# Kernel tuning notes

Measured on AMD Instinct MI355X. Metric: run time of the kernel, lower is better.

The kernel has to match this reference:

```python
import jax, jax.numpy as jnp
import numpy as np

B, G, DIN, DOUT = 4096, 16, 512, 512

def setup_inputs() -> dict:
    key = jax.random.key(0)
    kx, kw, kb = jax.random.split(key, 3)
    x = jax.random.normal(kx, (B, G, DIN), dtype=jnp.float32)
    # per-group nn.Linear weight: [G, dim_out, dim_in] (torch layout)
    W = jax.random.normal(kw, (G, DOUT, DIN), dtype=jnp.float32) * (1.0 / np.sqrt(DIN))
    b = jax.random.normal(kb, (G, DOUT), dtype=jnp.float32) * 0.01
    return {"x": x, "W": W, "b": b}

def reference(x, W, b):
    # MultiLinear: independent Linear per group g; y[..., g, :] = x[..., g, :] @ W[g].T + b[g]
    # Fused as a single batched GEMM over the group dimension.
    y = jnp.einsum('bgi,goi->bgo', x, W)  # [B, G, DOUT]
    return y + b
```

## Files before the change

kernel.cpp:

```cpp
#include <hip/hip_runtime.h>
#include <hip/hip_bf16.h>


#define BATCH 4096
#define NGRP  16
#define DIN   512
#define DOUT  512

#define BM 128
#define BN 512
#define BK 64
#define NT (DIN / BK)

typedef __bf16 bf16x8 __attribute__((ext_vector_type(8)));
typedef float  f32x4  __attribute__((ext_vector_type(4)));
typedef const __attribute__((address_space(1))) void gas_void;
typedef __attribute__((address_space(3))) void las_void;

__global__ __launch_bounds__(256)
void wcvt_kernel(const float* __restrict__ W, __bf16* __restrict__ Wb) {
    const int i = (blockIdx.x * 256 + threadIdx.x) * 8;
    f32x4 a = *(const f32x4*)(W + i);
    f32x4 b = *(const f32x4*)(W + i + 4);
    bf16x8 v;
#pragma unroll
    for (int j = 0; j < 4; ++j) { v[j] = (__bf16)a[j]; v[j + 4] = (__bf16)b[j]; }
    *(bf16x8*)(Wb + i) = v;
}

__global__ __launch_bounds__(512, 2)
void MultiLinear_48498770706571_kernel(const float* __restrict__ X,
                                       const __bf16* __restrict__ Wb,
                                       const float* __restrict__ Bias,
                                       float* __restrict__ Y) {
    const int bid = (blockIdx.x & 7) * 64 + (blockIdx.x >> 3);
    const int g   = bid >> 5;
    const int mt  = bid & 31;
    const int bm0 = mt * BM;

    __shared__ __bf16 As[2][BM * BK];
    __shared__ __bf16 BsF[2][BN * BK];

    const int tid  = threadIdx.x;
    const int lane = tid & 63;
    const int w    = tid >> 6;
    const int wn   = w * 64;
    const int l15  = lane & 15;
    const int q    = lane >> 4;

    const int srow = tid >> 2;
    const int sc2  = (tid & 3) * 2;
    const float* pA = X + (size_t)(bm0 + srow) * (NGRP * DIN) + g * DIN + (tid & 3) * 16;

    const int drow_l = lane >> 3;
    const int dch    = lane & 7;
    const __bf16* wbase = Wb + (size_t)g * (DOUT * DIN);

    f32x4 ra[4];

#define ISSUE_A(k0)                                                        \
    do {                                                                   \
        const f32x4* qa = (const f32x4*)(pA + (k0));                       \
        ra[0] = qa[0]; ra[1] = qa[1]; ra[2] = qa[2]; ra[3] = qa[3];        \
    } while (0)

#define CVT_WRITE_A(buf)                                                   \
    do {                                                                   \
        bf16x8 v0, v1;                                                     \
        _Pragma("unroll")                                                  \
        for (int j = 0; j < 4; ++j) {                                      \
            v0[j] = (__bf16)ra[0][j]; v0[j + 4] = (__bf16)ra[1][j];        \
            v1[j] = (__bf16)ra[2][j]; v1[j + 4] = (__bf16)ra[3][j];        \
        }                                                                  \
        const int s = srow & 7;                                            \
        __bf16* base = &As[buf][srow * BK];                                \
        *(bf16x8*)&base[((sc2 ^ s) << 3)]       = v0;                      \
        *(bf16x8*)&base[(((sc2 + 1) ^ s) << 3)] = v1;                      \
    } while (0)

#define DMA_B(kt, buf)                                                     \
    do {                                                                   \
        const size_t k0 = (size_t)(kt) * BK;                               \
        _Pragma("unroll")                                                  \
        for (int qq = 0; qq < 8; ++qq) {                                   \
            const int row = (w << 6) + (qq << 3) + drow_l;                 \
            const __bf16* gp = wbase + (size_t)row * DIN + k0              \
                               + ((dch ^ (row & 7)) << 3);                 \
            __builtin_amdgcn_global_load_lds(                              \
                (gas_void*)gp,                                             \
                (las_void*)&BsF[buf][(w << 12) + (qq << 9)], 16, 0, 0);    \
        }                                                                  \
    } while (0)

#define COMPUTE(buf)                                                       \
    do {                                                                   \
        _Pragma("unroll")                                                  \
        for (int kk = 0; kk < 2; ++kk) {                                   \
            bf16x8 af[8], bfr[4];                                          \
            _Pragma("unroll")                                              \
            for (int mi = 0; mi < 8; ++mi) {                               \
                const int row = mi * 16 + l15;                             \
                const int ch  = ((kk << 2) + q) ^ (row & 7);               \
                af[mi] = *(const bf16x8*)&As[buf][row * BK + (ch << 3)];   \
            }                                                              \
            _Pragma("unroll")                                              \
            for (int ni = 0; ni < 4; ++ni) {                               \
                const int brow = wn + ni * 16 + l15;                       \
                const int ch = ((kk << 2) + q) ^ (brow & 7);               \
                bfr[ni] = *(const bf16x8*)&BsF[buf][brow * BK + (ch << 3)]; \
            }                                                              \
            _Pragma("unroll")                                              \
            for (int mi = 0; mi < 8; ++mi)                                 \
                _Pragma("unroll")                                          \
                for (int ni = 0; ni < 4; ++ni)                             \
                    acc[mi][ni] = __builtin_amdgcn_mfma_f32_16x16x32_bf16( \
                        af[mi], bfr[ni], acc[mi][ni], 0, 0, 0);            \
        }                                                                  \
    } while (0)

    f32x4 acc[8][4];
#pragma unroll
    for (int mi = 0; mi < 8; ++mi)
#pragma unroll
        for (int ni = 0; ni < 4; ++ni) acc[mi][ni] = f32x4{0.f, 0.f, 0.f, 0.f};

    ISSUE_A(0);
    DMA_B(0, 0);
    CVT_WRITE_A(0);
    ISSUE_A(BK);

    for (int kt = 0; kt < NT; ++kt) {
        const int cur = kt & 1;
        if (kt + 1 < NT)
            asm volatile("s_waitcnt vmcnt(4)" ::: "memory");
        else
            asm volatile("s_waitcnt vmcnt(0)" ::: "memory");
        asm volatile("s_waitcnt lgkmcnt(0)" ::: "memory");
        __builtin_amdgcn_s_barrier();

        if (kt + 1 < NT) DMA_B(kt + 1, cur ^ 1);

        COMPUTE(cur);

        if (kt + 1 < NT) {
            CVT_WRITE_A(cur ^ 1);
            if (kt + 2 < NT) ISSUE_A((kt + 2) * BK);
        }
    }

    const int r0 = (lane >> 4) * 4;
    const int c  = lane & 15;
    float bias_n[4];
#pragma unroll
    for (int ni = 0; ni < 4; ++ni)
        bias_n[ni] = Bias[g * DOUT + wn + ni * 16 + c];
#pragma unroll
    for (int mi = 0; mi < 8; ++mi) {
#pragma unroll
        for (int j = 0; j < 4; ++j) {
            const int row = bm0 + mi * 16 + r0 + j;
            float* yrow = Y + (size_t)row * (NGRP * DOUT) + g * DOUT + wn;
#pragma unroll
            for (int ni = 0; ni < 4; ++ni)
                yrow[ni * 16 + c] = acc[mi][ni][j] + bias_n[ni];
        }
    }
#undef ISSUE_A
#undef CVT_WRITE_A
#undef DMA_B
#undef COMPUTE
}

extern "C" void kernel_launch(void* const* d_in, const int* in_sizes, int n_in,
                              void* d_out, int out_size, void* d_ws, size_t ws_size,
                              hipStream_t stream) {
    const float* X    = (const float*)d_in[0];
    const float* W    = (const float*)d_in[1];
    const float* Bias = (const float*)d_in[2];
    float* Y          = (float*)d_out;
    __bf16* Wb        = (__bf16*)d_ws;

    wcvt_kernel<<<2048, 256, 0, stream>>>(W, Wb);

    const int grid = NGRP * (BATCH / BM);
    MultiLinear_48498770706571_kernel<<<grid, 512, 0, stream>>>(X, Wb, Bias, Y);
}
```

Before: 73.80 us.

## Double the K tile to 128 and switch to single-buffered LDS staging

```diff
diff --git a/kernel.cpp b/kernel.cpp
--- a/kernel.cpp
+++ b/kernel.cpp
@@ -9,10 +9,11 @@
 
 #define BM 128
 #define BN 512
-#define BK 64
+#define BK 128
 #define NT (DIN / BK)
 
 typedef __bf16 bf16x8 __attribute__((ext_vector_type(8)));
+typedef __bf16 bf16x4 __attribute__((ext_vector_type(4)));
 typedef float  f32x4  __attribute__((ext_vector_type(4)));
 typedef const __attribute__((address_space(1))) void gas_void;
 typedef __attribute__((address_space(3))) void las_void;
@@ -38,8 +39,8 @@
     const int mt  = bid & 31;
     const int bm0 = mt * BM;
 
-    __shared__ __bf16 As[2][BM * BK];
-    __shared__ __bf16 BsF[2][BN * BK];
+    __shared__ __bf16 As[BM * BK];
+    __shared__ __bf16 BsF[BN * BK];
 
     const int tid  = threadIdx.x;
     const int lane = tid & 63;
@@ -49,65 +50,69 @@
     const int q    = lane >> 4;
 
     const int srow = tid >> 2;
-    const int sc2  = (tid & 3) * 2;
-    const float* pA = X + (size_t)(bm0 + srow) * (NGRP * DIN) + g * DIN + (tid & 3) * 16;
+    const int tq   = tid & 3;
+    const float* pA = X + (size_t)(bm0 + srow) * (NGRP * DIN) + g * DIN + tq * 4;
 
-    const int drow_l = lane >> 3;
-    const int dch    = lane & 7;
+    const int drow_l = lane >> 4;
+    const int dc     = lane & 15;
     const __bf16* wbase = Wb + (size_t)g * (DOUT * DIN);
 
-    f32x4 ra[4];
+    f32x4 ra[8];
 
 #define ISSUE_A(k0)                                                        \
     do {                                                                   \
-        const f32x4* qa = (const f32x4*)(pA + (k0));                       \
-        ra[0] = qa[0]; ra[1] = qa[1]; ra[2] = qa[2]; ra[3] = qa[3];        \
+        _Pragma("unroll")                                                  \
+        for (int j = 0; j < 8; ++j)                                        \
+            ra[j] = *(const f32x4*)(pA + (k0) + j * 16);                   \
     } while (0)
 
-#define CVT_WRITE_A(buf)                                                   \
+#define CVT_WRITE_A()                                                      \
     do {                                                                   \
-        bf16x8 v0, v1;                                                     \
+        const int s = srow & 7;                                            \
+        const int hb = (tq & 1) * 4;                                       \
         _Pragma("unroll")                                                  \
-        for (int j = 0; j < 4; ++j) {                                      \
-            v0[j] = (__bf16)ra[0][j]; v0[j + 4] = (__bf16)ra[1][j];        \
-            v1[j] = (__bf16)ra[2][j]; v1[j + 4] = (__bf16)ra[3][j];        \
+        for (int j = 0; j < 8; ++j) {                                      \
+            bf16x4 v;                                                      \
+            _Pragma("unroll")                                              \
+            for (int e = 0; e < 4; ++e) v[e] = (__bf16)ra[j][e];           \
+            const int lc   = j * 2 + (tq >> 1);                            \
+            const int phys = (lc & 8) | ((lc & 7) ^ s);                    \
+            *(bf16x4*)&As[srow * BK + phys * 8 + hb] = v;                  \
         }                                                                  \
-        const int s = srow & 7;                                            \
-        __bf16* base = &As[buf][srow * BK];                                \
-        *(bf16x8*)&base[((sc2 ^ s) << 3)]       = v0;                      \
-        *(bf16x8*)&base[(((sc2 + 1) ^ s) << 3)] = v1;                      \
     } while (0)
 
-#define DMA_B(kt, buf)                                                     \
+#define DMA_B(kt)                                                          \
     do {                                                                   \
         const size_t k0 = (size_t)(kt) * BK;                               \
         _Pragma("unroll")                                                  \
-        for (int qq = 0; qq < 8; ++qq) {                                   \
-            const int row = (w << 6) + (qq << 3) + drow_l;                 \
+        for (int qq = 0; qq < 16; ++qq) {                                  \
+            const int row  = (w << 6) + (qq << 2) + drow_l;                \
+            const int csrc = (dc & 8) | ((dc & 7) ^ (row & 7));            \
             const __bf16* gp = wbase + (size_t)row * DIN + k0              \
-                               + ((dch ^ (row & 7)) << 3);                 \
+                               + (csrc << 3);                              \
             __builtin_amdgcn_global_load_lds(                              \
                 (gas_void*)gp,                                             \
-                (las_void*)&BsF[buf][(w << 12) + (qq << 9)], 16, 0, 0);    \
+                (las_void*)&BsF[((w << 6) + (qq << 2)) * BK], 16, 0, 0);   \
         }                                                                  \
     } while (0)
 
-#define COMPUTE(buf)                                                       \
+#define COMPUTE()                                                          \
     do {                                                                   \
         _Pragma("unroll")                                                  \
-        for (int kk = 0; kk < 2; ++kk) {                                   \
+        for (int kk = 0; kk < 4; ++kk) {                                   \
             bf16x8 af[8], bfr[4];                                          \
+            const int chl = (kk << 2) + q;                                 \
             _Pragma("unroll")                                              \
             for (int mi = 0; mi < 8; ++mi) {                               \
-                const int row = mi * 16 + l15;                             \
-                const int ch  = ((kk << 2) + q) ^ (row & 7);               \
-                af[mi] = *(const bf16x8*)&As[buf][row * BK + (ch << 3)];   \
+                const int row  = mi * 16 + l15;                            \
+                const int phys = (chl & 8) | ((chl & 7) ^ (row & 7));      \
+                af[mi] = *(const bf16x8*)&As[row * BK + (phys << 3)];      \
             }                                                              \
             _Pragma("unroll")                                              \
             for (int ni = 0; ni < 4; ++ni) {                               \
                 const int brow = wn + ni * 16 + l15;                       \
-                const int ch = ((kk << 2) + q) ^ (brow & 7);               \
-                bfr[ni] = *(const bf16x8*)&BsF[buf][brow * BK + (ch << 3)]; \
+                const int phys = (chl & 8) | ((chl & 7) ^ (brow & 7));     \
+                bfr[ni] = *(const bf16x8*)&BsF[brow * BK + (phys << 3)];   \
             }                                                              \
             _Pragma("unroll")                                              \
             for (int mi = 0; mi < 8; ++mi)                                 \
@@ -125,26 +130,28 @@
         for (int ni = 0; ni < 4; ++ni) acc[mi][ni] = f32x4{0.f, 0.f, 0.f, 0.f};
 
     ISSUE_A(0);
-    DMA_B(0, 0);
-    CVT_WRITE_A(0);
+    DMA_B(0);
+    CVT_WRITE_A();
     ISSUE_A(BK);
+    asm volatile("s_waitcnt lgkmcnt(0)" ::: "memory");
+    __builtin_amdgcn_s_barrier();
 
     for (int kt = 0; kt < NT; ++kt) {
-        const int cur = kt & 1;
         if (kt + 1 < NT)
-            asm volatile("s_waitcnt vmcnt(4)" ::: "memory");
+            asm volatile("s_waitcnt vmcnt(8)" ::: "memory");
         else
             asm volatile("s_waitcnt vmcnt(0)" ::: "memory");
-        asm volatile("s_waitcnt lgkmcnt(0)" ::: "memory");
-        __builtin_amdgcn_s_barrier();
 
-        if (kt + 1 < NT) DMA_B(kt + 1, cur ^ 1);
-
-        COMPUTE(cur);
+        COMPUTE();
 
         if (kt + 1 < NT) {
-            CVT_WRITE_A(cur ^ 1);
+            asm volatile("s_waitcnt lgkmcnt(0)" ::: "memory");
+            __builtin_amdgcn_s_barrier();
+            DMA_B(kt + 1);
+            CVT_WRITE_A();
             if (kt + 2 < NT) ISSUE_A((kt + 2) * BK);
+            asm volatile("s_waitcnt lgkmcnt(0)" ::: "memory");
+            __builtin_amdgcn_s_barrier();
         }
     }
 
```

Measured after the change: 84.67 us. +14.7%, slower.
